# Kernel tuning notes

Measured on AMD Instinct MI355X. Metric: run time of the kernel, lower is better.

The kernel has to match this reference:

```python
import jax, jax.numpy as jnp
import numpy as np

N = 100000      # nodes
E = 1600000     # edges (avg degree 16)
IN, HID, OUT = 128, 32, 16
H = 2           # attention heads
EPS = 1e-5
NEG_SLOPE = 0.2


def setup_inputs() -> dict:
    key = jax.random.key(0)
    ks = jax.random.split(key, 24)
    f32 = jnp.float32
    def w(k, shape, scale=0.1):
        return jax.random.normal(k, shape, f32) * scale
    return {
        "x": jax.random.normal(ks[0], (N, IN), f32),
        "edge_index": jax.random.randint(ks[1], (2, E), 0, N, dtype=jnp.int32),
        # GCN layer 1
        "gcn1_W": w(ks[2], (IN, HID)), "gcn1_b": w(ks[3], (HID,)),
        # BN1 (eval mode: running stats)
        "bn1_g": 1.0 + w(ks[4], (HID,)), "bn1_b": w(ks[5], (HID,)),
        "bn1_m": w(ks[6], (HID,)), "bn1_v": 1.0 + jnp.abs(w(ks[7], (HID,))),
        # GAT layer 1 (HID -> HID, heads=H, concat=False)
        "gat1_W": w(ks[8], (HID, H * HID)), "gat1_as": w(ks[9], (H, HID)),
        "gat1_ad": w(ks[10], (H, HID)), "gat1_b": w(ks[11], (HID,)),
        # GCN layer 2
        "gcn2_W": w(ks[12], (HID, HID)), "gcn2_b": w(ks[13], (HID,)),
        # BN2
        "bn2_g": 1.0 + w(ks[14], (HID,)), "bn2_b": w(ks[15], (HID,)),
        "bn2_m": w(ks[16], (HID,)), "bn2_v": 1.0 + jnp.abs(w(ks[17], (HID,))),
        # GAT layer 2 (HID -> OUT, heads=H, concat=False)
        "gat2_W": w(ks[18], (HID, H * OUT)), "gat2_as": w(ks[19], (H, OUT)),
        "gat2_ad": w(ks[20], (H, OUT)), "gat2_b": w(ks[21], (OUT,)),
    }


def _add_self_loops(edge_index):
    loop = jnp.arange(N, dtype=edge_index.dtype)
    src = jnp.concatenate([edge_index[0], loop])
    dst = jnp.concatenate([edge_index[1], loop])
    return src, dst


def _gcn(x, src, dst, W, b):
    h = x @ W                                             # [N, F]
    deg = jax.ops.segment_sum(jnp.ones_like(dst, h.dtype), dst, N)
    dinv = jax.lax.rsqrt(jnp.maximum(deg, 1.0))
    norm = dinv[src] * dinv[dst]                          # [Etot]
    out = jax.ops.segment_sum(h[src] * norm[:, None], dst, N)
    return out + b


def _gat(x, src, dst, W, a_src, a_dst, b, F):
    # PyG GATConv (concat=False -> mean over heads); eval mode (no attn dropout)
    h = (x @ W).reshape(N, H, F)                          # [N, H, F]
    al_s = jnp.einsum('nhf,hf->nh', h, a_src)             # [N, H]
    al_d = jnp.einsum('nhf,hf->nh', h, a_dst)
    e = jax.nn.leaky_relu(al_s[src] + al_d[dst], NEG_SLOPE)  # [Etot, H]
    # segment softmax over destination neighborhoods (self-loops ensure >=1 edge)
    m = jax.ops.segment_max(e, dst, N)
    ex = jnp.exp(e - m[dst])
    s = jax.ops.segment_sum(ex, dst, N)
    alpha = ex / s[dst]                                   # [Etot, H]
    out = jax.ops.segment_sum(alpha[:, :, None] * h[src], dst, N)  # [N, H, F]
    return out.mean(axis=1) + b


def _bn_eval(x, g, b, m, v):
    return (x - m) * jax.lax.rsqrt(v + EPS) * g + b


def reference(x, edge_index, gcn1_W, gcn1_b, bn1_g, bn1_b, bn1_m, bn1_v,
              gat1_W, gat1_as, gat1_ad, gat1_b, gcn2_W, gcn2_b,
              bn2_g, bn2_b, bn2_m, bn2_v, gat2_W, gat2_as, gat2_ad, gat2_b):
    src, dst = _add_self_loops(edge_index)
    h = _gcn(x, src, dst, gcn1_W, gcn1_b)
    h = jax.nn.relu(_bn_eval(h, bn1_g, bn1_b, bn1_m, bn1_v))
    h = jax.nn.relu(_gat(h, src, dst, gat1_W, gat1_as, gat1_ad, gat1_b, HID))
    h = _gcn(h, src, dst, gcn2_W, gcn2_b)
    h = jax.nn.relu(_bn_eval(h, bn2_g, bn2_b, bn2_m, bn2_v))
    h = _gat(h, src, dst, gat2_W, gat2_as, gat2_ad, gat2_b, OUT)
    return jax.nn.log_softmax(h, axis=1)
```

## Files before the change

kernel.cpp:

```cpp
#include <hip/hip_runtime.h>
#include <hip/hip_bf16.h>

#define NN 100000
#define EE 1600000
#define SLAB 64
#define KB 391
#define CHUNK 4096
#define BSLAB 4736

static constexpr float EPSV = 1e-5f;
static constexpr float SLOPE = 0.2f;

__device__ __forceinline__ float lrelu(float v) { return v > 0.f ? v : SLOPE * v; }

__device__ __forceinline__ unsigned rne_bf16(float v) {
    unsigned u = __float_as_uint(v);
    return (u + 0x7fffu + ((u >> 16) & 1u)) >> 16;
}
__device__ __forceinline__ float bf16_lo(unsigned u) { return __uint_as_float(u << 16); }
__device__ __forceinline__ float bf16_hi(unsigned u) { return __uint_as_float(u & 0xffff0000u); }


__global__ void k_z(int* __restrict__ bcnt, unsigned* __restrict__ hsp,
                    unsigned* __restrict__ g1p, unsigned* __restrict__ g2p) {
    int i = threadIdx.x;
    if (i < KB) bcnt[i] = 0;
    if (i < 16) hsp[(size_t)NN * 16 + i] = 0u;
    if (i < 32) g1p[(size_t)NN * 32 + i] = 0u;
    if (i < 16) g2p[(size_t)NN * 16 + i] = 0u;
}

__global__ __launch_bounds__(256) void k_scat(const int* __restrict__ src, const int* __restrict__ dst,
                                              int* __restrict__ bcnt, unsigned int* __restrict__ ebuf) {
    __shared__ int hc[KB], hb[KB];
    int tid = threadIdx.x;
    for (int i = tid; i < KB; i += 256) hc[i] = 0;
    __syncthreads();
    int e0 = blockIdx.x * CHUNK;
    #pragma unroll
    for (int r = 0; r < CHUNK / 256; ++r) {
        int e = e0 + r * 256 + tid;
        if (e < EE) atomicAdd(&hc[dst[e] >> 8], 1);
    }
    __syncthreads();
    for (int i = tid; i < KB; i += 256) {
        int c = hc[i];
        if (c) hb[i] = atomicAdd(&bcnt[i], c);
        hc[i] = 0;
    }
    __syncthreads();
    #pragma unroll
    for (int r = 0; r < CHUNK / 256; ++r) {
        int e = e0 + r * 256 + tid;
        if (e < EE) {
            int d = dst[e];
            int b = d >> 8;
            int rk = atomicAdd(&hc[b], 1);
            ebuf[(size_t)b * BSLAB + hb[b] + rk] = ((unsigned)src[e] << 8) | (unsigned)(d & 255);
        }
    }
}

__global__ __launch_bounds__(256) void k_bucket(const unsigned int* __restrict__ ebuf,
                                                const int* __restrict__ bcnt,
                                                int* __restrict__ col, int* __restrict__ cnt) {
    __shared__ int lc[256];
    int tid = threadIdx.x;
    int b = blockIdx.x;
    lc[tid] = 0;
    __syncthreads();
    size_t s = (size_t)b * BSLAB;
    int nb = bcnt[b];
    for (int i = tid; i < nb; i += 256) {
        unsigned v = ebuf[s + i];
        int l = v & 255;
        int r = atomicAdd(&lc[l], 1);
        col[(((b << 8) + l) << 6) + r] = v >> 8;
    }
    __syncthreads();
    int node = (b << 8) + tid;
    if (node < NN) cnt[node] = lc[tid];
}

__global__ void k_deg(const int* __restrict__ cnt, float* __restrict__ dinv,
                      int* __restrict__ col) {
    int i = blockIdx.x * 256 + threadIdx.x;
    if (i < NN) {
        int c = cnt[i];
        dinv[i] = rsqrtf((float)(c + 1));
        col[i * SLAB + c] = i;
        for (int j = c + 1; j < 32; ++j) col[i * SLAB + j] = NN;
    }
}


__global__ __launch_bounds__(256) void k_gemm1(const float* __restrict__ x,
                                               const float* __restrict__ W,
                                               const float* __restrict__ dinv,
                                               unsigned* __restrict__ hsp) {
    __shared__ float xs[64][128];
    int tid = threadIdx.x;
    int lane = tid & 63;
    int wv = tid >> 6;
    int khalf = lane >> 5, f = lane & 31;
    float wreg[64];
    const float* wp = W + (khalf * 64) * 32 + f;
    #pragma unroll
    for (int i = 0; i < 64; ++i) wreg[i] = wp[i * 32];
    int n0 = blockIdx.x * 64;
    for (int i = tid; i < 64 * 32; i += 256) {
        int row = i >> 5, c4 = i & 31;
        int n = n0 + row;
        float4 v = (n < NN) ? *(const float4*)&x[(size_t)n * 128 + c4 * 4]
                            : make_float4(0.f, 0.f, 0.f, 0.f);
        *(float4*)&xs[row][c4 * 4] = v;
    }
    __syncthreads();
    #pragma unroll 4
    for (int t = 0; t < 16; ++t) {
        int row = wv * 16 + t;
        int n = n0 + row;
        if (n >= NN) break;
        const float* xp = &xs[row][khalf * 64];
        float a0 = 0.f, a1 = 0.f, a2 = 0.f, a3 = 0.f;
        #pragma unroll
        for (int j = 0; j < 16; j += 4) {
            float4 v0 = *(const float4*)&xp[(j + 0) * 4];
            float4 v1 = *(const float4*)&xp[(j + 1) * 4];
            float4 v2 = *(const float4*)&xp[(j + 2) * 4];
            float4 v3 = *(const float4*)&xp[(j + 3) * 4];
            a0 += v0.x * wreg[j * 4 + 0]  + v0.y * wreg[j * 4 + 1]  + v0.z * wreg[j * 4 + 2]  + v0.w * wreg[j * 4 + 3];
            a1 += v1.x * wreg[j * 4 + 4]  + v1.y * wreg[j * 4 + 5]  + v1.z * wreg[j * 4 + 6]  + v1.w * wreg[j * 4 + 7];
            a2 += v2.x * wreg[j * 4 + 8]  + v2.y * wreg[j * 4 + 9]  + v2.z * wreg[j * 4 + 10] + v2.w * wreg[j * 4 + 11];
            a3 += v3.x * wreg[j * 4 + 12] + v3.y * wreg[j * 4 + 13] + v3.z * wreg[j * 4 + 14] + v3.w * wreg[j * 4 + 15];
        }
        float tot = (a0 + a1) + (a2 + a3);
        tot += __shfl_xor(tot, 32);
        unsigned r16 = rne_bf16(tot * dinv[n]);
        unsigned hi16 = __shfl(r16, f + 1, 32);
        if (khalf == 0 && !(f & 1))
            hsp[n * 16 + (f >> 1)] = (hi16 << 16) | (r16 & 0xffffu);
    }
}

__device__ __forceinline__ float quad_sum_hsp(const unsigned* hsp, int c0, int lane) {
    int q = lane & 7, sub = lane >> 3;
    const uint2* h2 = (const uint2*)hsp;
    float ac0 = 0.f, ac1 = 0.f, ac2 = 0.f, ac3 = 0.f;
    #pragma unroll
    for (int s = 0; s < 8; ++s) {
        int c = __shfl(c0, 4 * s + sub, 32);
        uint2 u = h2[(size_t)c * 8 + q];
        ac0 += bf16_lo(u.x); ac1 += bf16_hi(u.x);
        ac2 += bf16_lo(u.y); ac3 += bf16_hi(u.y);
    }
    ac0 += __shfl_xor(ac0, 8); ac0 += __shfl_xor(ac0, 16);
    ac1 += __shfl_xor(ac1, 8); ac1 += __shfl_xor(ac1, 16);
    ac2 += __shfl_xor(ac2, 8); ac2 += __shfl_xor(ac2, 16);
    ac3 += __shfl_xor(ac3, 8); ac3 += __shfl_xor(ac3, 16);
    int p = lane >> 2;
    float v0 = __shfl(ac0, p, 32), v1 = __shfl(ac1, p, 32);
    float v2 = __shfl(ac2, p, 32), v3 = __shfl(ac3, p, 32);
    float s01 = (lane & 1) ? v1 : v0;
    float s23 = (lane & 1) ? v3 : v2;
    return (lane & 2) ? s23 : s01;
}

__device__ __forceinline__ float gen_sum_hsp(const unsigned* hsp, const int* col, int base,
                                             int dn, int lane) {
    int half = lane >> 4, l16 = lane & 15;
    int c0 = col[base + lane];
    int c1 = col[base + 32 + lane];
    float aL0 = 0.f, aH0 = 0.f, aL1 = 0.f, aH1 = 0.f;
    for (int j2 = 0; j2 < dn; j2 += 4) {
        int eA = j2 + half, eB = j2 + 2 + half;
        int cA = __shfl((j2 < 32) ? c0 : c1, eA & 31, 32);
        int cB = __shfl((j2 + 2 < 32) ? c0 : c1, eB & 31, 32);
        bool okA = eA < dn, okB = eB < dn;
        unsigned uA = hsp[(okA ? cA : 0) * 16 + l16];
        unsigned uB = hsp[(okB ? cB : 0) * 16 + l16];
        uA = okA ? uA : 0u; uB = okB ? uB : 0u;
        aL0 += bf16_lo(uA); aH0 += bf16_hi(uA);
        aL1 += bf16_lo(uB); aH1 += bf16_hi(uB);
    }
    float accLo = aL0 + aL1, accHi = aH0 + aH1;
    accLo += __shfl_xor(accLo, 16);
    accHi += __shfl_xor(accHi, 16);
    float vLo = __shfl(accLo, lane >> 1, 32);
    float vHi = __shfl(accHi, lane >> 1, 32);
    return (lane & 1) ? vHi : vLo;
}


__global__ __launch_bounds__(256) void k_gcn1_gat1t(
    const unsigned* __restrict__ hsp, const int* __restrict__ cnt,
    const int* __restrict__ col, const float* __restrict__ dinv,
    const float* __restrict__ gb, const float* __restrict__ bng,
    const float* __restrict__ bnb, const float* __restrict__ bnm,
    const float* __restrict__ bnv,
    const float* __restrict__ W1, const float* __restrict__ as_, const float* __restrict__ ad_,
    unsigned* __restrict__ gp, float* __restrict__ al) {
    __shared__ float wAs[32][32], wBs[32][32];
    int tid = threadIdx.x;
    for (int i = tid; i < 1024; i += 256) {
        int k = i >> 5, f = i & 31;
        wAs[k][f] = W1[k * 64 + f];
        wBs[k][f] = W1[k * 64 + 32 + f];
    }
    __syncthreads();
    int r = tid >> 5, lane = tid & 31;
    int n = blockIdx.x * 8 + r;
    int dn = cnt[n] + 1;
    int base = n * SLAB;
    float acc;
    if (dn <= 32) acc = quad_sum_hsp(hsp, col[base + lane], lane);
    else          acc = gen_sum_hsp(hsp, col, base, dn, lane);
    float v = dinv[n] * acc + gb[lane];
    v = (v - bnm[lane]) * rsqrtf(bnv[lane] + EPSV) * bng[lane] + bnb[lane];
    v = fmaxf(v, 0.f);
    float gA0 = 0.f, gA1 = 0.f, gB0 = 0.f, gB1 = 0.f;
    #pragma unroll
    for (int k = 0; k < 32; k += 2) {
        float t0 = __shfl(v, k, 32);
        float t1v = __shfl(v, k + 1, 32);
        gA0 += t0 * wAs[k][lane];     gB0 += t0 * wBs[k][lane];
        gA1 += t1v * wAs[k + 1][lane]; gB1 += t1v * wBs[k + 1][lane];
    }
    float gA = gA0 + gA1, gB = gB0 + gB1;
    float pas0 = gA * as_[lane],      pad0 = gA * ad_[lane];
    float pas1 = gB * as_[32 + lane], pad1 = gB * ad_[32 + lane];
    #pragma unroll
    for (int off = 16; off; off >>= 1) {
        pas0 += __shfl_xor(pas0, off);
        pad0 += __shfl_xor(pad0, off);
        pas1 += __shfl_xor(pas1, off);
        pad1 += __shfl_xor(pad1, off);
    }
    if (lane == 0) *(float4*)&al[n * 4] = make_float4(pas0, pas1, pad0, pad1);
    gp[n * 32 + lane] = (rne_bf16(gB) << 16) | rne_bf16(gA);
}


__global__ __launch_bounds__(256) void k_gat1_pv(
    const unsigned* __restrict__ gp, const float* __restrict__ al,
    const int* __restrict__ cnt, const int* __restrict__ col,
    const float* __restrict__ b, const float* __restrict__ W2,
    const float* __restrict__ dinv, unsigned* __restrict__ hs3p) {
    __shared__ float2 ec[8][SLAB];
    __shared__ float w2s[32][32];
    int tid = threadIdx.x;
    for (int i = tid; i < 1024; i += 256) w2s[i >> 5][i & 31] = W2[i];
    __syncthreads();
    int r = tid >> 5, lane = tid & 31;
    int n = blockIdx.x * 8 + r;
    int dn = cnt[n] + 1;
    int base = n * SLAB;
    int c0 = col[base + lane];
    int c1 = (dn > 32) ? col[base + 32 + lane] : (int)NN;
    float ad0 = al[n * 4 + 2], ad1 = al[n * 4 + 3];
    float e0a = -1e30f, e1a = -1e30f, e0b = -1e30f, e1b = -1e30f;
    if (lane < dn) {
        float4 a4 = *(const float4*)&al[(size_t)c0 * 4];
        e0a = lrelu(a4.x + ad0); e1a = lrelu(a4.y + ad1);
    }
    if (32 + lane < dn) {
        float4 a4 = *(const float4*)&al[(size_t)c1 * 4];
        e0b = lrelu(a4.x + ad0); e1b = lrelu(a4.y + ad1);
    }
    float m0 = fmaxf(e0a, e0b), m1 = fmaxf(e1a, e1b);
    #pragma unroll
    for (int off = 16; off; off >>= 1) {
        m0 = fmaxf(m0, __shfl_xor(m0, off));
        m1 = fmaxf(m1, __shfl_xor(m1, off));
    }
    float x0a = (lane < dn) ? __expf(e0a - m0) : 0.f;
    float x1a = (lane < dn) ? __expf(e1a - m1) : 0.f;
    float x0b = (32 + lane < dn) ? __expf(e0b - m0) : 0.f;
    float x1b = (32 + lane < dn) ? __expf(e1b - m1) : 0.f;
    ec[r][lane] = make_float2(x0a, x1a);
    ec[r][32 + lane] = make_float2(x0b, x1b);
    float s0 = x0a + x0b, s1 = x1a + x1b;
    #pragma unroll
    for (int off = 16; off; off >>= 1) {
        s0 += __shfl_xor(s0, off);
        s1 += __shfl_xor(s1, off);
    }
    float A0, A1;
    if (dn <= 32) {
        int q = lane & 7, sub = lane >> 3;
        const uint4* g4 = (const uint4*)gp;
        float aL0 = 0.f, aL1 = 0.f, aL2 = 0.f, aL3 = 0.f;
        float aH0 = 0.f, aH1 = 0.f, aH2 = 0.f, aH3 = 0.f;
        #pragma unroll
        for (int s = 0; s < 8; ++s) {
            int e = 4 * s + sub;
            int c = __shfl(c0, e, 32);
            uint4 u = g4[(size_t)c * 8 + q];
            float2 wv = ec[r][e];
            aL0 += wv.x * bf16_lo(u.x); aH0 += wv.y * bf16_hi(u.x);
            aL1 += wv.x * bf16_lo(u.y); aH1 += wv.y * bf16_hi(u.y);
            aL2 += wv.x * bf16_lo(u.z); aH2 += wv.y * bf16_hi(u.z);
            aL3 += wv.x * bf16_lo(u.w); aH3 += wv.y * bf16_hi(u.w);
        }
        aL0 += __shfl_xor(aL0, 8); aL0 += __shfl_xor(aL0, 16);
        aL1 += __shfl_xor(aL1, 8); aL1 += __shfl_xor(aL1, 16);
        aL2 += __shfl_xor(aL2, 8); aL2 += __shfl_xor(aL2, 16);
        aL3 += __shfl_xor(aL3, 8); aL3 += __shfl_xor(aL3, 16);
        aH0 += __shfl_xor(aH0, 8); aH0 += __shfl_xor(aH0, 16);
        aH1 += __shfl_xor(aH1, 8); aH1 += __shfl_xor(aH1, 16);
        aH2 += __shfl_xor(aH2, 8); aH2 += __shfl_xor(aH2, 16);
        aH3 += __shfl_xor(aH3, 8); aH3 += __shfl_xor(aH3, 16);
        int p = lane >> 2;
        float l0 = __shfl(aL0, p, 32), l1 = __shfl(aL1, p, 32);
        float l2 = __shfl(aL2, p, 32), l3 = __shfl(aL3, p, 32);
        float h0 = __shfl(aH0, p, 32), h1 = __shfl(aH1, p, 32);
        float h2 = __shfl(aH2, p, 32), h3 = __shfl(aH3, p, 32);
        float sl01 = (lane & 1) ? l1 : l0, sl23 = (lane & 1) ? l3 : l2;
        float sh01 = (lane & 1) ? h1 : h0, sh23 = (lane & 1) ? h3 : h2;
        A0 = (lane & 2) ? sl23 : sl01;
        A1 = (lane & 2) ? sh23 : sh01;
    } else {
        int half = lane >> 4, l16 = lane & 15;
        const uint2* gp2 = (const uint2*)gp;
        float a0L = 0.f, a0H = 0.f, a1L = 0.f, a1H = 0.f;
        float b0L = 0.f, b0H = 0.f, b1L = 0.f, b1H = 0.f;
        for (int j2 = 0; j2 < dn; j2 += 4) {
            int eA = j2 + half, eB = j2 + 2 + half;
            int cA = __shfl((j2 < 32) ? c0 : c1, eA & 31, 32);
            int cB = __shfl((j2 + 2 < 32) ? c0 : c1, eB & 31, 32);
            bool okA = eA < dn, okB = eB < dn;
            uint2 uA = gp2[(size_t)(okA ? cA : 0) * 16 + l16];
            uint2 uB = gp2[(size_t)(okB ? cB : 0) * 16 + l16];
            float2 wA = ec[r][eA & 63];
            float2 wB = ec[r][eB & 63];
            uA.x = okA ? uA.x : 0u; uA.y = okA ? uA.y : 0u;
            uB.x = okB ? uB.x : 0u; uB.y = okB ? uB.y : 0u;
            a0L += wA.x * bf16_lo(uA.x); a1L += wA.y * bf16_hi(uA.x);
            a0H += wA.x * bf16_lo(uA.y); a1H += wA.y * bf16_hi(uA.y);
            b0L += wB.x * bf16_lo(uB.x); b1L += wB.y * bf16_hi(uB.x);
            b0H += wB.x * bf16_lo(uB.y); b1H += wB.y * bf16_hi(uB.y);
        }
        a0L += b0L; a0H += b0H; a1L += b1L; a1H += b1H;
        a0L += __shfl_xor(a0L, 16); a0H += __shfl_xor(a0H, 16);
        a1L += __shfl_xor(a1L, 16); a1H += __shfl_xor(a1H, 16);
        int p = lane >> 1;
        float t0L = __shfl(a0L, p, 32), t0H = __shfl(a0H, p, 32);
        float t1L = __shfl(a1L, p, 32), t1H = __shfl(a1H, p, 32);
        A0 = (lane & 1) ? t0H : t0L;
        A1 = (lane & 1) ? t1H : t1L;
    }
    float v = 0.5f * (A0 / s0 + A1 / s1) + b[lane];
    v = fmaxf(v, 0.f);
    float g0 = 0.f, g1 = 0.f;
    #pragma unroll
    for (int k = 0; k < 32; k += 2) {
        g0 += __shfl(v, k, 32) * w2s[k][lane];
        g1 += __shfl(v, k + 1, 32) * w2s[k + 1][lane];
    }
    unsigned r16 = rne_bf16((g0 + g1) * dinv[n]);
    unsigned hi16 = __shfl(r16, lane + 1, 32);
    if (!(lane & 1)) hs3p[n * 16 + (lane >> 1)] = (hi16 << 16) | (r16 & 0xffffu);
}


__global__ __launch_bounds__(256) void k_gcn2_gat2t(
    const unsigned* __restrict__ hsp, const int* __restrict__ cnt,
    const int* __restrict__ col, const float* __restrict__ dinv,
    const float* __restrict__ gb, const float* __restrict__ bng,
    const float* __restrict__ bnb, const float* __restrict__ bnm,
    const float* __restrict__ bnv,
    const float* __restrict__ Wg, const float* __restrict__ as_, const float* __restrict__ ad_,
    unsigned* __restrict__ g2p, float* __restrict__ al) {
    __shared__ float wgs[32][32];
    int tid = threadIdx.x;
    for (int i = tid; i < 1024; i += 256) wgs[i >> 5][i & 31] = Wg[i];
    __syncthreads();
    int r = tid >> 5, lane = tid & 31;
    int n = blockIdx.x * 8 + r;
    int dn = cnt[n] + 1;
    int base = n * SLAB;
    float acc;
    if (dn <= 32) acc = quad_sum_hsp(hsp, col[base + lane], lane);
    else          acc = gen_sum_hsp(hsp, col, base, dn, lane);
    float v = dinv[n] * acc + gb[lane];
    v = (v - bnm[lane]) * rsqrtf(bnv[lane] + EPSV) * bng[lane] + bnb[lane];
    v = fmaxf(v, 0.f);
    float g0 = 0.f, g1 = 0.f;
    #pragma unroll
    for (int k = 0; k < 32; k += 2) {
        g0 += __shfl(v, k, 32) * wgs[k][lane];
        g1 += __shfl(v, k + 1, 32) * wgs[k + 1][lane];
    }
    float g = g0 + g1;
    int hh = lane >> 4, ff = lane & 15;
    float as_v = g * as_[hh * 16 + ff];
    float ad_v = g * ad_[hh * 16 + ff];
    #pragma unroll
    for (int off = 8; off; off >>= 1) {
        as_v += __shfl_xor(as_v, off);
        ad_v += __shfl_xor(ad_v, off);
    }
    if (ff == 0) { al[n * 4 + hh] = as_v; al[n * 4 + 2 + hh] = ad_v; }
    unsigned r16 = rne_bf16(g);
    unsigned hi16 = __shfl(r16, lane + 1, 32);
    if (!(lane & 1)) g2p[n * 16 + (lane >> 1)] = (hi16 << 16) | (r16 & 0xffffu);
}


__global__ __launch_bounds__(256) void k_gat2_agg(
    const unsigned* __restrict__ g2p, const float* __restrict__ al,
    const int* __restrict__ cnt, const int* __restrict__ col,
    const float* __restrict__ b, float* __restrict__ out) {
    __shared__ float2 ec[8][SLAB];
    int tid = threadIdx.x;
    int r = tid >> 5, lane = tid & 31;
    int n = blockIdx.x * 8 + r;
    int dn = cnt[n] + 1;
    int base = n * SLAB;
    int c0 = col[base + lane];
    int c1 = (dn > 32) ? col[base + 32 + lane] : (int)NN;
    float ad0 = al[n * 4 + 2], ad1 = al[n * 4 + 3];
    float e0a = -1e30f, e1a = -1e30f, e0b = -1e30f, e1b = -1e30f;
    if (lane < dn) {
        float4 a4 = *(const float4*)&al[(size_t)c0 * 4];
        e0a = lrelu(a4.x + ad0); e1a = lrelu(a4.y + ad1);
    }
    if (32 + lane < dn) {
        float4 a4 = *(const float4*)&al[(size_t)c1 * 4];
        e0b = lrelu(a4.x + ad0); e1b = lrelu(a4.y + ad1);
    }
    float m0 = fmaxf(e0a, e0b), m1 = fmaxf(e1a, e1b);
    #pragma unroll
    for (int off = 16; off; off >>= 1) {
        m0 = fmaxf(m0, __shfl_xor(m0, off));
        m1 = fmaxf(m1, __shfl_xor(m1, off));
    }
    float x0a = (lane < dn) ? __expf(e0a - m0) : 0.f;
    float x1a = (lane < dn) ? __expf(e1a - m1) : 0.f;
    float x0b = (32 + lane < dn) ? __expf(e0b - m0) : 0.f;
    float x1b = (32 + lane < dn) ? __expf(e1b - m1) : 0.f;
    ec[r][lane] = make_float2(x0a, x1a);
    ec[r][32 + lane] = make_float2(x0b, x1b);
    float s0 = x0a + x0b, s1 = x1a + x1b;
    #pragma unroll
    for (int off = 16; off; off >>= 1) {
        s0 += __shfl_xor(s0, off);
        s1 += __shfl_xor(s1, off);
    }
    float acc;
    if (dn <= 32) {
        int q = lane & 7, sub = lane >> 3;
        bool head1 = (lane & 4) != 0;
        const uint2* g2 = (const uint2*)g2p;
        float ac0 = 0.f, ac1 = 0.f, ac2 = 0.f, ac3 = 0.f;
        #pragma unroll
        for (int s = 0; s < 8; ++s) {
            int e = 4 * s + sub;
            int c = __shfl(c0, e, 32);
            uint2 u = g2[(size_t)c * 8 + q];
            float2 wv = ec[r][e];
            float w = head1 ? wv.y : wv.x;
            ac0 += w * bf16_lo(u.x); ac1 += w * bf16_hi(u.x);
            ac2 += w * bf16_lo(u.y); ac3 += w * bf16_hi(u.y);
        }
        ac0 += __shfl_xor(ac0, 8); ac0 += __shfl_xor(ac0, 16);
        ac1 += __shfl_xor(ac1, 8); ac1 += __shfl_xor(ac1, 16);
        ac2 += __shfl_xor(ac2, 8); ac2 += __shfl_xor(ac2, 16);
        ac3 += __shfl_xor(ac3, 8); ac3 += __shfl_xor(ac3, 16);
        int p = lane >> 2;
        float v0 = __shfl(ac0, p, 32), v1 = __shfl(ac1, p, 32);
        float v2 = __shfl(ac2, p, 32), v3 = __shfl(ac3, p, 32);
        float s01 = (lane & 1) ? v1 : v0;
        float s23 = (lane & 1) ? v3 : v2;
        acc = (lane & 2) ? s23 : s01;
    } else {
        int half = lane >> 4, l16 = lane & 15;
        bool head1g = (l16 & 8) != 0;
        float aL0 = 0.f, aH0 = 0.f, aL1 = 0.f, aH1 = 0.f;
        for (int j2 = 0; j2 < dn; j2 += 4) {
            int eA = j2 + half, eB = j2 + 2 + half;
            int cA = __shfl((j2 < 32) ? c0 : c1, eA & 31, 32);
            int cB = __shfl((j2 + 2 < 32) ? c0 : c1, eB & 31, 32);
            bool okA = eA < dn, okB = eB < dn;
            unsigned uA = g2p[(okA ? cA : 0) * 16 + l16];
            unsigned uB = g2p[(okB ? cB : 0) * 16 + l16];
            float2 wA = ec[r][eA & 63];
            float2 wB = ec[r][eB & 63];
            float wa = head1g ? wA.y : wA.x;
            float wb = head1g ? wB.y : wB.x;
            uA = okA ? uA : 0u; uB = okB ? uB : 0u;
            aL0 += wa * bf16_lo(uA); aH0 += wa * bf16_hi(uA);
            aL1 += wb * bf16_lo(uB); aH1 += wb * bf16_hi(uB);
        }
        float accLo = aL0 + aL1, accHi = aH0 + aH1;
        accLo += __shfl_xor(accLo, 16);
        accHi += __shfl_xor(accHi, 16);
        float vLo = __shfl(accLo, lane >> 1, 32);
        float vHi = __shfl(accHi, lane >> 1, 32);
        acc = (lane & 1) ? vHi : vLo;
    }
    int hh = lane >> 4, ff = lane & 15;
    acc /= (hh ? s1 : s0);
    float v = 0.5f * (acc + __shfl_xor(acc, 16)) + b[ff];
    float mx = v;
    #pragma unroll
    for (int off = 8; off; off >>= 1) mx = fmaxf(mx, __shfl_xor(mx, off));
    float se = __expf(v - mx);
    #pragma unroll
    for (int off = 8; off; off >>= 1) se += __shfl_xor(se, off);
    if (hh == 0) out[(size_t)n * 16 + ff] = v - mx - __logf(se);
}


static inline size_t al256(size_t x) { return (x + 255) & ~((size_t)255); }

extern "C" void kernel_launch(void* const* d_in, const int* in_sizes, int n_in,
                              void* d_out, int out_size, void* d_ws, size_t ws_size,
                              hipStream_t stream) {
    const float* x      = (const float*)d_in[0];
    const int*   ei     = (const int*)d_in[1];
    const float* gcn1_W = (const float*)d_in[2];
    const float* gcn1_b = (const float*)d_in[3];
    const float* bn1_g  = (const float*)d_in[4];
    const float* bn1_b  = (const float*)d_in[5];
    const float* bn1_m  = (const float*)d_in[6];
    const float* bn1_v  = (const float*)d_in[7];
    const float* gat1_W = (const float*)d_in[8];
    const float* gat1_as= (const float*)d_in[9];
    const float* gat1_ad= (const float*)d_in[10];
    const float* gat1_b = (const float*)d_in[11];
    const float* gcn2_W = (const float*)d_in[12];
    const float* gcn2_b = (const float*)d_in[13];
    const float* bn2_g  = (const float*)d_in[14];
    const float* bn2_b  = (const float*)d_in[15];
    const float* bn2_m  = (const float*)d_in[16];
    const float* bn2_v  = (const float*)d_in[17];
    const float* gat2_W = (const float*)d_in[18];
    const float* gat2_as= (const float*)d_in[19];
    const float* gat2_ad= (const float*)d_in[20];
    const float* gat2_b = (const float*)d_in[21];
    float* out = (float*)d_out;

    char* w = (char*)d_ws;
    size_t off = 0;
    auto alloc = [&](size_t bytes) { void* p = w + off; off = al256(off + bytes); return p; };
    int*      cnt   = (int*)alloc((size_t)NN * 4);
    float*    dinv  = (float*)alloc((size_t)NN * 4);
    int*      col   = (int*)alloc((size_t)NN * SLAB * 4);
    unsigned* hsp   = (unsigned*)alloc((size_t)(NN + 1) * 16 * 4);
    unsigned* g1p   = (unsigned*)alloc((size_t)(NN + 1) * 32 * 4);
    unsigned* g2p   = (unsigned*)alloc((size_t)(NN + 1) * 16 * 4);
    float*    al    = (float*)alloc((size_t)NN * 4 * 4);
    int*      bcnt  = (int*)alloc((size_t)KB * 4);
    unsigned int* ebuf = (unsigned int*)g1p;

    const int* esrc = ei;
    const int* edst = ei + EE;
    const int GE = (EE + CHUNK - 1) / CHUNK;

    k_z<<<1, 512, 0, stream>>>(bcnt, hsp, g1p, g2p);
    k_scat<<<GE, 256, 0, stream>>>(esrc, edst, bcnt, ebuf);
    k_bucket<<<KB, 256, 0, stream>>>(ebuf, bcnt, col, cnt);
    k_deg<<<(NN + 255) / 256, 256, 0, stream>>>(cnt, dinv, col);

    k_gemm1<<<(NN + 63) / 64, 256, 0, stream>>>(x, gcn1_W, dinv, hsp);
    k_gcn1_gat1t<<<NN / 8, 256, 0, stream>>>(hsp, cnt, col, dinv, gcn1_b,
                                             bn1_g, bn1_b, bn1_m, bn1_v,
                                             gat1_W, gat1_as, gat1_ad, g1p, al);
    k_gat1_pv<<<NN / 8, 256, 0, stream>>>(g1p, al, cnt, col, gat1_b,
                                          gcn2_W, dinv, hsp);
    k_gcn2_gat2t<<<NN / 8, 256, 0, stream>>>(hsp, cnt, col, dinv, gcn2_b,
                                             bn2_g, bn2_b, bn2_m, bn2_v,
                                             gat2_W, gat2_as, gat2_ad, g2p, al);
    k_gat2_agg<<<NN / 8, 256, 0, stream>>>(g2p, al, cnt, col, gat2_b, out);
}
```

Baseline: 280.8 us.

## Fuse degree kernel into bucket and prefetch neighbor gathers before weight staging

Merges the separate degree/padding kernel into the bucket kernel, removing one launch and a reread of cnt. In the per-node aggregation kernels, the neighbor feature gathers for the common low-degree case are issued into registers before the shared-memory weight staging and softmax, so gather latency overlaps with that work. Softmax weights in the common path are broadcast via shuffles instead of a shared-memory round trip. This raises register pressure, which may reduce occupancy.

```diff
diff --git a/kernel.cpp b/kernel.cpp
--- a/kernel.cpp
+++ b/kernel.cpp
@@ -63,7 +63,8 @@
 
 __global__ __launch_bounds__(256) void k_bucket(const unsigned int* __restrict__ ebuf,
                                                 const int* __restrict__ bcnt,
-                                                int* __restrict__ col, int* __restrict__ cnt) {
+                                                int* __restrict__ col, int* __restrict__ cnt,
+                                                float* __restrict__ dinv) {
     __shared__ int lc[256];
     int tid = threadIdx.x;
     int b = blockIdx.x;
@@ -79,17 +80,12 @@
     }
     __syncthreads();
     int node = (b << 8) + tid;
-    if (node < NN) cnt[node] = lc[tid];
-}
-
-__global__ void k_deg(const int* __restrict__ cnt, float* __restrict__ dinv,
-                      int* __restrict__ col) {
-    int i = blockIdx.x * 256 + threadIdx.x;
-    if (i < NN) {
-        int c = cnt[i];
-        dinv[i] = rsqrtf((float)(c + 1));
-        col[i * SLAB + c] = i;
-        for (int j = c + 1; j < 32; ++j) col[i * SLAB + j] = NN;
+    if (node < NN) {
+        int c = lc[tid];
+        cnt[node] = c;
+        dinv[node] = rsqrtf((float)(c + 1));
+        col[node * SLAB + c] = node;
+        for (int j = c + 1; j < 32; ++j) col[node * SLAB + j] = NN;
     }
 }
 
@@ -143,16 +139,12 @@
     }
 }
 
-__device__ __forceinline__ float quad_sum_hsp(const unsigned* hsp, int c0, int lane) {
-    int q = lane & 7, sub = lane >> 3;
-    const uint2* h2 = (const uint2*)hsp;
+__device__ __forceinline__ float quad_reduce_u2(const uint2* u, int lane) {
     float ac0 = 0.f, ac1 = 0.f, ac2 = 0.f, ac3 = 0.f;
     #pragma unroll
     for (int s = 0; s < 8; ++s) {
-        int c = __shfl(c0, 4 * s + sub, 32);
-        uint2 u = h2[(size_t)c * 8 + q];
-        ac0 += bf16_lo(u.x); ac1 += bf16_hi(u.x);
-        ac2 += bf16_lo(u.y); ac3 += bf16_hi(u.y);
+        ac0 += bf16_lo(u[s].x); ac1 += bf16_hi(u[s].x);
+        ac2 += bf16_lo(u[s].y); ac3 += bf16_hi(u[s].y);
     }
     ac0 += __shfl_xor(ac0, 8); ac0 += __shfl_xor(ac0, 16);
     ac1 += __shfl_xor(ac1, 8); ac1 += __shfl_xor(ac1, 16);
@@ -202,19 +194,31 @@
     unsigned* __restrict__ gp, float* __restrict__ al) {
     __shared__ float wAs[32][32], wBs[32][32];
     int tid = threadIdx.x;
+    int r = tid >> 5, lane = tid & 31;
+    int n = blockIdx.x * 8 + r;
+    int dn = cnt[n] + 1;
+    int base = n * SLAB;
+    int c0 = col[base + lane];
+    bool common = (dn <= 32);
+    uint2 u[8];
+    if (common) {
+        int q = lane & 7, sub = lane >> 3;
+        const uint2* h2 = (const uint2*)hsp;
+        #pragma unroll
+        for (int s = 0; s < 8; ++s) {
+            int c = __shfl(c0, 4 * s + sub, 32);
+            u[s] = h2[(size_t)c * 8 + q];
+        }
+    }
     for (int i = tid; i < 1024; i += 256) {
         int k = i >> 5, f = i & 31;
         wAs[k][f] = W1[k * 64 + f];
         wBs[k][f] = W1[k * 64 + 32 + f];
     }
     __syncthreads();
-    int r = tid >> 5, lane = tid & 31;
-    int n = blockIdx.x * 8 + r;
-    int dn = cnt[n] + 1;
-    int base = n * SLAB;
     float acc;
-    if (dn <= 32) acc = quad_sum_hsp(hsp, col[base + lane], lane);
-    else          acc = gen_sum_hsp(hsp, col, base, dn, lane);
+    if (common) acc = quad_reduce_u2(u, lane);
+    else        acc = gen_sum_hsp(hsp, col, base, dn, lane);
     float v = dinv[n] * acc + gb[lane];
     v = (v - bnm[lane]) * rsqrtf(bnv[lane] + EPSV) * bng[lane] + bnb[lane];
     v = fmaxf(v, 0.f);
@@ -249,14 +253,24 @@
     __shared__ float2 ec[8][SLAB];
     __shared__ float w2s[32][32];
     int tid = threadIdx.x;
-    for (int i = tid; i < 1024; i += 256) w2s[i >> 5][i & 31] = W2[i];
-    __syncthreads();
     int r = tid >> 5, lane = tid & 31;
     int n = blockIdx.x * 8 + r;
     int dn = cnt[n] + 1;
     int base = n * SLAB;
     int c0 = col[base + lane];
     int c1 = (dn > 32) ? col[base + 32 + lane] : (int)NN;
+    bool common = (dn <= 32);
+    uint4 u[8];
+    if (common) {
+        int q = lane & 7, sub = lane >> 3;
+        const uint4* g4 = (const uint4*)gp;
+        #pragma unroll
+        for (int s = 0; s < 8; ++s) {
+            int c = __shfl(c0, 4 * s + sub, 32);
+            u[s] = g4[(size_t)c * 8 + q];
+        }
+    }
+    for (int i = tid; i < 1024; i += 256) w2s[i >> 5][i & 31] = W2[i];
     float ad0 = al[n * 4 + 2], ad1 = al[n * 4 + 3];
     float e0a = -1e30f, e1a = -1e30f, e0b = -1e30f, e1b = -1e30f;
     if (lane < dn) {
@@ -277,8 +291,6 @@
     float x1a = (lane < dn) ? __expf(e1a - m1) : 0.f;
     float x0b = (32 + lane < dn) ? __expf(e0b - m0) : 0.f;
     float x1b = (32 + lane < dn) ? __expf(e1b - m1) : 0.f;
-    ec[r][lane] = make_float2(x0a, x1a);
-    ec[r][32 + lane] = make_float2(x0b, x1b);
     float s0 = x0a + x0b, s1 = x1a + x1b;
     #pragma unroll
     for (int off = 16; off; off >>= 1) {
@@ -286,21 +298,19 @@
         s1 += __shfl_xor(s1, off);
     }
     float A0, A1;
-    if (dn <= 32) {
-        int q = lane & 7, sub = lane >> 3;
-        const uint4* g4 = (const uint4*)gp;
+    if (common) {
+        int sub = lane >> 3;
         float aL0 = 0.f, aL1 = 0.f, aL2 = 0.f, aL3 = 0.f;
         float aH0 = 0.f, aH1 = 0.f, aH2 = 0.f, aH3 = 0.f;
         #pragma unroll
         for (int s = 0; s < 8; ++s) {
             int e = 4 * s + sub;
-            int c = __shfl(c0, e, 32);
-            uint4 u = g4[(size_t)c * 8 + q];
-            float2 wv = ec[r][e];
-            aL0 += wv.x * bf16_lo(u.x); aH0 += wv.y * bf16_hi(u.x);
-            aL1 += wv.x * bf16_lo(u.y); aH1 += wv.y * bf16_hi(u.y);
-            aL2 += wv.x * bf16_lo(u.z); aH2 += wv.y * bf16_hi(u.z);
-            aL3 += wv.x * bf16_lo(u.w); aH3 += wv.y * bf16_hi(u.w);
+            float w0 = __shfl(x0a, e, 32);
+            float w1 = __shfl(x1a, e, 32);
+            aL0 += w0 * bf16_lo(u[s].x); aH0 += w1 * bf16_hi(u[s].x);
+            aL1 += w0 * bf16_lo(u[s].y); aH1 += w1 * bf16_hi(u[s].y);
+            aL2 += w0 * bf16_lo(u[s].z); aH2 += w1 * bf16_hi(u[s].z);
+            aL3 += w0 * bf16_lo(u[s].w); aH3 += w1 * bf16_hi(u[s].w);
         }
         aL0 += __shfl_xor(aL0, 8); aL0 += __shfl_xor(aL0, 16);
         aL1 += __shfl_xor(aL1, 8); aL1 += __shfl_xor(aL1, 16);
@@ -320,6 +330,8 @@
         A0 = (lane & 2) ? sl23 : sl01;
         A1 = (lane & 2) ? sh23 : sh01;
     } else {
+        ec[r][lane] = make_float2(x0a, x1a);
+        ec[r][32 + lane] = make_float2(x0b, x1b);
         int half = lane >> 4, l16 = lane & 15;
         const uint2* gp2 = (const uint2*)gp;
         float a0L = 0.f, a0H = 0.f, a1L = 0.f, a1H = 0.f;
@@ -349,6 +361,7 @@
         A0 = (lane & 1) ? t0H : t0L;
         A1 = (lane & 1) ? t1H : t1L;
     }
+    __syncthreads();
     float v = 0.5f * (A0 / s0 + A1 / s1) + b[lane];
     v = fmaxf(v, 0.f);
     float g0 = 0.f, g1 = 0.f;
@@ -373,15 +386,27 @@
     unsigned* __restrict__ g2p, float* __restrict__ al) {
     __shared__ float wgs[32][32];
     int tid = threadIdx.x;
-    for (int i = tid; i < 1024; i += 256) wgs[i >> 5][i & 31] = Wg[i];
-    __syncthreads();
     int r = tid >> 5, lane = tid & 31;
     int n = blockIdx.x * 8 + r;
     int dn = cnt[n] + 1;
     int base = n * SLAB;
+    int c0 = col[base + lane];
+    bool common = (dn <= 32);
+    uint2 u[8];
+    if (common) {
+        int q = lane & 7, sub = lane >> 3;
+        const uint2* h2 = (const uint2*)hsp;
+        #pragma unroll
+        for (int s = 0; s < 8; ++s) {
+            int c = __shfl(c0, 4 * s + sub, 32);
+            u[s] = h2[(size_t)c * 8 + q];
+        }
+    }
+    for (int i = tid; i < 1024; i += 256) wgs[i >> 5][i & 31] = Wg[i];
+    __syncthreads();
     float acc;
-    if (dn <= 32) acc = quad_sum_hsp(hsp, col[base + lane], lane);
-    else          acc = gen_sum_hsp(hsp, col, base, dn, lane);
+    if (common) acc = quad_reduce_u2(u, lane);
+    else        acc = gen_sum_hsp(hsp, col, base, dn, lane);
     float v = dinv[n] * acc + gb[lane];
     v = (v - bnm[lane]) * rsqrtf(bnv[lane] + EPSV) * bng[lane] + bnb[lane];
     v = fmaxf(v, 0.f);
@@ -419,6 +444,17 @@
     int base = n * SLAB;
     int c0 = col[base + lane];
     int c1 = (dn > 32) ? col[base + 32 + lane] : (int)NN;
+    bool common = (dn <= 32);
+    uint2 u[8];
+    if (common) {
+        int q = lane & 7, sub = lane >> 3;
+        const uint2* g2 = (const uint2*)g2p;
+        #pragma unroll
+        for (int s = 0; s < 8; ++s) {
+            int c = __shfl(c0, 4 * s + sub, 32);
+            u[s] = g2[(size_t)c * 8 + q];
+        }
+    }
     float ad0 = al[n * 4 + 2], ad1 = al[n * 4 + 3];
     float e0a = -1e30f, e1a = -1e30f, e0b = -1e30f, e1b = -1e30f;
     if (lane < dn) {
@@ -439,8 +475,6 @@
     float x1a = (lane < dn) ? __expf(e1a - m1) : 0.f;
     float x0b = (32 + lane < dn) ? __expf(e0b - m0) : 0.f;
     float x1b = (32 + lane < dn) ? __expf(e1b - m1) : 0.f;
-    ec[r][lane] = make_float2(x0a, x1a);
-    ec[r][32 + lane] = make_float2(x0b, x1b);
     float s0 = x0a + x0b, s1 = x1a + x1b;
     #pragma unroll
     for (int off = 16; off; off >>= 1) {
@@ -448,20 +482,18 @@
         s1 += __shfl_xor(s1, off);
     }
     float acc;
-    if (dn <= 32) {
-        int q = lane & 7, sub = lane >> 3;
+    if (common) {
+        int sub = lane >> 3;
         bool head1 = (lane & 4) != 0;
-        const uint2* g2 = (const uint2*)g2p;
         float ac0 = 0.f, ac1 = 0.f, ac2 = 0.f, ac3 = 0.f;
         #pragma unroll
         for (int s = 0; s < 8; ++s) {
             int e = 4 * s + sub;
-            int c = __shfl(c0, e, 32);
-            uint2 u = g2[(size_t)c * 8 + q];
-            float2 wv = ec[r][e];
-            float w = head1 ? wv.y : wv.x;
-            ac0 += w * bf16_lo(u.x); ac1 += w * bf16_hi(u.x);
-            ac2 += w * bf16_lo(u.y); ac3 += w * bf16_hi(u.y);
+            float w0 = __shfl(x0a, e, 32);
+            float w1 = __shfl(x1a, e, 32);
+            float w = head1 ? w1 : w0;
+            ac0 += w * bf16_lo(u[s].x); ac1 += w * bf16_hi(u[s].x);
+            ac2 += w * bf16_lo(u[s].y); ac3 += w * bf16_hi(u[s].y);
         }
         ac0 += __shfl_xor(ac0, 8); ac0 += __shfl_xor(ac0, 16);
         ac1 += __shfl_xor(ac1, 8); ac1 += __shfl_xor(ac1, 16);
@@ -474,6 +506,8 @@
         float s23 = (lane & 1) ? v3 : v2;
         acc = (lane & 2) ? s23 : s01;
     } else {
+        ec[r][lane] = make_float2(x0a, x1a);
+        ec[r][32 + lane] = make_float2(x0b, x1b);
         int half = lane >> 4, l16 = lane & 15;
         bool head1g = (l16 & 8) != 0;
         float aL0 = 0.f, aH0 = 0.f, aL1 = 0.f, aH1 = 0.f;
@@ -560,8 +594,7 @@
 
     k_z<<<1, 512, 0, stream>>>(bcnt, hsp, g1p, g2p);
     k_scat<<<GE, 256, 0, stream>>>(esrc, edst, bcnt, ebuf);
-    k_bucket<<<KB, 256, 0, stream>>>(ebuf, bcnt, col, cnt);
-    k_deg<<<(NN + 255) / 256, 256, 0, stream>>>(cnt, dinv, col);
+    k_bucket<<<KB, 256, 0, stream>>>(ebuf, bcnt, col, cnt, dinv);
 
     k_gemm1<<<(NN + 63) / 64, 256, 0, stream>>>(x, gcn1_W, dinv, hsp);
     k_gcn1_gat1t<<<NN / 8, 256, 0, stream>>>(hsp, cnt, col, dinv, gcn1_b,
```

Result: slower. 287.9 us (+2.5%).
